# Optimization experiments

Hardware: AMD Instinct MI355X
Metric: run time of the kernel (lower is better)

Reference implementation:

```python
import jax, jax.numpy as jnp
import numpy as np

EMBED = 8      # embed_dim channels of 32-blade multivectors
HIDDEN = 32    # hidden_dim channels
BLADES = 32    # 2^5 Clifford blades
DT = 0.01


def setup_inputs() -> dict:
    key = jax.random.key(0)
    ks = jax.random.split(key, 8)
    B, S, N, D = 32, 256, 16, 6
    scale = lambda k, shape: jax.random.normal(k, shape, jnp.float32) * 0.1
    return {
        "x": jax.random.normal(ks[0], (B, S, N, D), jnp.float32),
        # input_proj: Linear(6, embed_dim*32)
        "W_in": scale(ks[1], (D, EMBED * BLADES)),
        "b_in": jnp.zeros((EMBED * BLADES,), jnp.float32),
        # VersorLinear(embed, hidden): channel-mixing weight shared across blades, per-blade bias
        "W1": scale(ks[2], (HIDDEN, EMBED)),
        "b1": scale(ks[3], (HIDDEN, BLADES)),
        "W2": scale(ks[4], (HIDDEN, HIDDEN)),
        "b2": scale(ks[5], (HIDDEN, BLADES)),
        "W3": scale(ks[6], (1, HIDDEN)),
        "b3": scale(ks[7], (1, BLADES)),
    }


def _versor_linear(h, W, b):
    # h: [..., in_ch, 32 blades]; mix channels, shared over blades
    return jnp.einsum('...ik,oi->...ok', h, W) + b


def _versor_act(h):
    # gate each multivector channel by sigmoid of its scalar (blade-0) part
    return h * jax.nn.sigmoid(h[..., 0:1])


def _energy(x_flat, W_in, b_in, W1, b1, W2, b2, W3, b3):
    BS, N, D = x_flat.shape
    h = x_flat @ W_in + b_in                    # [BS, N, EMBED*32]
    h = h.reshape(BS, N, EMBED, BLADES)         # [BS, N, embed, 32]
    h = _versor_act(_versor_linear(h, W1, b1))
    h = _versor_act(_versor_linear(h, W2, b2))
    h = _versor_linear(h, W3, b3)               # [BS, N, 1, 32]
    return h[..., 0].sum()                      # scalar energy


def reference(x, W_in, b_in, W1, b1, W2, b2, W3, b3):
    B, S, N, D = x.shape
    x_flat = x.reshape(B * S, N, D)
    # symplectic gradient of the Hamiltonian w.r.t. state
    grads = jax.grad(_energy)(x_flat, W_in, b_in, W1, b1, W2, b2, W3, b3)
    dq_dt = grads[..., 3:]
    dp_dt = -grads[..., :3]
    next_state = x_flat + jnp.concatenate([dq_dt, dp_dt], axis=-1) * DT
    return next_state.reshape(B, S, N, D)
```

## Files before the change

kernel.cpp:

```cpp
#include <hip/hip_runtime.h>
#include <hip/hip_bf16.h>

#define DT_STEP 0.01f

typedef __bf16 bf16x8 __attribute__((ext_vector_type(8)));
typedef float  f32x4  __attribute__((ext_vector_type(4)));

#define OFF_W2   0
#define OFF_W1   4096
#define OFF_WIND 5120
#define OFF_BIND 5312
#define OFF_B1D  5344
#define OFF_B2D  5472
#define OFF_W3   5600
#define OFF_WE   5728
#define OFF_BE   6496
#define OFF_WCP  6624
#define OFF_WAVE 7680
#define LDS_TOTAL (7680 + 4*3072)

__device__ __forceinline__ bf16x8 readT(const char* buf, int l15, int lhi) {
    return *(const bf16x8*)(buf + ((l15 * 64 + lhi * 16) ^ ((l15 & 7) << 4)));
}

__device__ __forceinline__ void act_sw(const f32x4& p0, const f32x4& p1,
                                       float* t0, float* t1, char* buf, int l15, int lhi) {
#pragma unroll
    for (int e = 0; e < 4; ++e) {
        int s = lhi * 4 + e, m = (s & 7) << 4;
        float a = p0[e], g = 1.f / (1.f + __expf(-a));
        t0[e] = g * fmaf(a, 1.f - g, 1.f);
        *(__bf16*)(buf + ((s * 64 + l15 * 2) ^ m)) = (__bf16)(a * g);
        a = p1[e]; g = 1.f / (1.f + __expf(-a));
        t1[e] = g * fmaf(a, 1.f - g, 1.f);
        *(__bf16*)(buf + ((s * 64 + (l15 + 16) * 2) ^ m)) = (__bf16)(a * g);
    }
}

__device__ __forceinline__ void d2_sw(const f32x4& p0, const f32x4& p1,
                                      float w30, float w31, char* buf, int l15, int lhi) {
#pragma unroll
    for (int e = 0; e < 4; ++e) {
        int s = lhi * 4 + e, m = (s & 7) << 4;
        float a = p0[e], g = 1.f / (1.f + __expf(-a));
        *(__bf16*)(buf + ((s * 64 + l15 * 2) ^ m)) = (__bf16)(w30 * g * fmaf(a, 1.f - g, 1.f));
        a = p1[e]; g = 1.f / (1.f + __expf(-a));
        *(__bf16*)(buf + ((s * 64 + (l15 + 16) * 2) ^ m)) = (__bf16)(w31 * g * fmaf(a, 1.f - g, 1.f));
    }
}

__device__ __forceinline__ void d1_sw(const f32x4& u0, const f32x4& u1,
                                      const float* t0, const float* t1, char* buf, int l15, int lhi) {
#pragma unroll
    for (int e = 0; e < 4; ++e) {
        int s = lhi * 4 + e, m = (s & 7) << 4;
        *(__bf16*)(buf + ((s * 64 + l15 * 2) ^ m))        = (__bf16)(u0[e] * t0[e]);
        *(__bf16*)(buf + ((s * 64 + (l15 + 16) * 2) ^ m)) = (__bf16)(u1[e] * t1[e]);
    }
}

__global__ __launch_bounds__(256) void hvnn_fused(
    const float* __restrict__ x,
    const float* __restrict__ Win, const float* __restrict__ bin,
    const float* __restrict__ W1,  const float* __restrict__ b1,
    const float* __restrict__ W2,  const float* __restrict__ b2,
    const float* __restrict__ W3,
    float* __restrict__ out, int ntiles)
{
    __shared__ __align__(16) char lds[LDS_TOTAL];
    const int tid = threadIdx.x;
    const int lane = tid & 63, wv = tid >> 6;
    const int l15 = lane & 15, lhi = lane >> 4;

    const int tileA = blockIdx.x * 8 + wv;
    const int tileB = tileA + 4;
    const bool vA = tileA < ntiles, vB = tileB < ntiles;

    char* wbase = lds + OFF_WAVE + wv * 3072;
    char* bufA = wbase;         char* bufB = wbase + 1024;
    char* xA   = wbase + 2048;  char* xB   = wbase + 2560;

    if (lane < 48) {
        if (vA) *(float2*)(xA + lane * 8) = ((const float2*)x)[(size_t)tileA * 48 + lane];
        if (vB) *(float2*)(xB + lane * 8) = ((const float2*)x)[(size_t)tileB * 48 + lane];
    }

    ((float4*)(lds + OFF_W2))[tid] = ((const float4*)W2)[tid];
    ((float*)(lds + OFF_W1))[tid]  = W1[tid];
    if (tid < 48) ((float*)(lds + OFF_WIND))[tid] = Win[(tid >> 3) * 256 + (tid & 7) * 32];
    if (tid < 8)  ((float*)(lds + OFF_BIND))[tid] = bin[tid * 32];
    if (tid < 32) ((float*)(lds + OFF_B1D))[tid]  = b1[tid * 32];
    if (tid < 32) ((float*)(lds + OFF_B2D))[tid]  = b2[tid * 32];
    if (tid < 32) ((float*)(lds + OFF_W3))[tid]   = W3[tid];
    __syncthreads();

    const float* W1s  = (const float*)(lds + OFF_W1);
    const float* Wind = (const float*)(lds + OFF_WIND);
    if (tid < 192) {
        int d = tid >> 5, o = tid & 31;
        float a = 0.f;
#pragma unroll
        for (int i = 0; i < 8; ++i) a = fmaf(Wind[d * 8 + i], W1s[o * 8 + i], a);
        ((float*)(lds + OFF_WE))[d * 32 + o] = a;
    }
    if (tid < 32) {
        float a = ((const float*)(lds + OFF_B1D))[tid];
#pragma unroll
        for (int i = 0; i < 8; ++i) a = fmaf(((const float*)(lds + OFF_BIND))[i], W1s[tid * 8 + i], a);
        ((float*)(lds + OFF_BE))[tid] = a;
    }
    {
        int o = tid >> 3, d = tid & 7;
        float v = 0.f;
        if (d < 6) {
            int dd = d < 3 ? d + 3 : d - 3;
            float sg = d < 3 ? 1.f : -1.f;
            float a = 0.f;
#pragma unroll
            for (int i = 0; i < 8; ++i) a = fmaf(W1s[o * 8 + i], Wind[dd * 8 + i], a);
            v = sg * a;
        }
        ((float*)(lds + OFF_WCP))[o * 8 + d] = v;
    }
    __syncthreads();

    const float* WeS  = (const float*)(lds + OFF_WE);
    const float* W2s  = (const float*)(lds + OFF_W2);
    const float* WcpS = (const float*)(lds + OFF_WCP);
    bf16x8 bwe0 = {}, bwe1 = {}, bw2t0, bw2t1, bw2b0, bw2b1, bwc = {};
    if (lane < 16) {
#pragma unroll
        for (int d = 0; d < 6; ++d) {
            bwe0[d] = (__bf16)WeS[d * 32 + l15];
            bwe1[d] = (__bf16)WeS[d * 32 + l15 + 16];
        }
    }
#pragma unroll
    for (int j = 0; j < 8; ++j) {
        bw2t0[j] = (__bf16)W2s[l15 * 32 + lhi * 8 + j];
        bw2t1[j] = (__bf16)W2s[(l15 + 16) * 32 + lhi * 8 + j];
        bw2b0[j] = (__bf16)W2s[(lhi * 8 + j) * 32 + l15];
        bw2b1[j] = (__bf16)W2s[(lhi * 8 + j) * 32 + l15 + 16];
    }
    if (l15 < 6) {
#pragma unroll
        for (int j = 0; j < 8; ++j) bwc[j] = (__bf16)WcpS[(lhi * 8 + j) * 8 + l15];
    }
    const float be0  = ((const float*)(lds + OFF_BE))[l15];
    const float be1  = ((const float*)(lds + OFF_BE))[l15 + 16];
    const float b2c0 = ((const float*)(lds + OFF_B2D))[l15];
    const float b2c1 = ((const float*)(lds + OFF_B2D))[l15 + 16];
    const float w3c0 = ((const float*)(lds + OFF_W3))[l15];
    const float w3c1 = ((const float*)(lds + OFF_W3))[l15 + 16];

    bf16x8 axA = {}, axB = {};
    if (lane < 16) {
        const float* ra = (const float*)(xA + lane * 24);
        const float* rb = (const float*)(xB + lane * 24);
#pragma unroll
        for (int d = 0; d < 6; ++d) { axA[d] = (__bf16)ra[d]; axB[d] = (__bf16)rb[d]; }
    }

    const f32x4 c0 = {be0, be0, be0, be0}, c1 = {be1, be1, be1, be1};
    f32x4 h1p0A = __builtin_amdgcn_mfma_f32_16x16x32_bf16(axA, bwe0, c0, 0, 0, 0);
    f32x4 h1p1A = __builtin_amdgcn_mfma_f32_16x16x32_bf16(axA, bwe1, c1, 0, 0, 0);
    f32x4 h1p0B = __builtin_amdgcn_mfma_f32_16x16x32_bf16(axB, bwe0, c0, 0, 0, 0);
    f32x4 h1p1B = __builtin_amdgcn_mfma_f32_16x16x32_bf16(axB, bwe1, c1, 0, 0, 0);

    float t10A[4], t11A[4], t10B[4], t11B[4];
    act_sw(h1p0A, h1p1A, t10A, t11A, bufA, l15, lhi);
    act_sw(h1p0B, h1p1B, t10B, t11B, bufB, l15, lhi);
    bf16x8 h1aA = readT(bufA, l15, lhi);
    bf16x8 h1aB = readT(bufB, l15, lhi);

    const f32x4 cb0 = {b2c0, b2c0, b2c0, b2c0}, cb1 = {b2c1, b2c1, b2c1, b2c1};
    f32x4 h2p0A = __builtin_amdgcn_mfma_f32_16x16x32_bf16(h1aA, bw2t0, cb0, 0, 0, 0);
    f32x4 h2p1A = __builtin_amdgcn_mfma_f32_16x16x32_bf16(h1aA, bw2t1, cb1, 0, 0, 0);
    f32x4 h2p0B = __builtin_amdgcn_mfma_f32_16x16x32_bf16(h1aB, bw2t0, cb0, 0, 0, 0);
    f32x4 h2p1B = __builtin_amdgcn_mfma_f32_16x16x32_bf16(h1aB, bw2t1, cb1, 0, 0, 0);

    d2_sw(h2p0A, h2p1A, w3c0, w3c1, bufA, l15, lhi);
    d2_sw(h2p0B, h2p1B, w3c0, w3c1, bufB, l15, lhi);
    bf16x8 d2aA = readT(bufA, l15, lhi);
    bf16x8 d2aB = readT(bufB, l15, lhi);

    const f32x4 z = {0.f, 0.f, 0.f, 0.f};
    f32x4 u10A = __builtin_amdgcn_mfma_f32_16x16x32_bf16(d2aA, bw2b0, z, 0, 0, 0);
    f32x4 u11A = __builtin_amdgcn_mfma_f32_16x16x32_bf16(d2aA, bw2b1, z, 0, 0, 0);
    f32x4 u10B = __builtin_amdgcn_mfma_f32_16x16x32_bf16(d2aB, bw2b0, z, 0, 0, 0);
    f32x4 u11B = __builtin_amdgcn_mfma_f32_16x16x32_bf16(d2aB, bw2b1, z, 0, 0, 0);

    d1_sw(u10A, u11A, t10A, t11A, bufA, l15, lhi);
    d1_sw(u10B, u11B, t10B, t11B, bufB, l15, lhi);
    bf16x8 d1aA = readT(bufA, l15, lhi);
    bf16x8 d1aB = readT(bufB, l15, lhi);

    f32x4 gxA = __builtin_amdgcn_mfma_f32_16x16x32_bf16(d1aA, bwc, z, 0, 0, 0);
    f32x4 gxB = __builtin_amdgcn_mfma_f32_16x16x32_bf16(d1aB, bwc, z, 0, 0, 0);

    if (l15 < 6) {
#pragma unroll
        for (int e = 0; e < 4; ++e) {
            int di = (lhi * 4 + e) * 6 + l15;
            *(float*)(bufA + di * 4) = fmaf(DT_STEP, gxA[e], *(const float*)(xA + di * 4));
            *(float*)(bufB + di * 4) = fmaf(DT_STEP, gxB[e], *(const float*)(xB + di * 4));
        }
    }
    if (lane < 48) {
        if (vA) ((float2*)out)[(size_t)tileA * 48 + lane] = *(const float2*)(bufA + lane * 8);
        if (vB) ((float2*)out)[(size_t)tileB * 48 + lane] = *(const float2*)(bufB + lane * 8);
    }
}

extern "C" void kernel_launch(void* const* d_in, const int* in_sizes, int n_in,
                              void* d_out, int out_size, void* d_ws, size_t ws_size,
                              hipStream_t stream) {
    const float* x    = (const float*)d_in[0];
    const float* W_in = (const float*)d_in[1];
    const float* b_in = (const float*)d_in[2];
    const float* W1   = (const float*)d_in[3];
    const float* b1   = (const float*)d_in[4];
    const float* W2   = (const float*)d_in[5];
    const float* b2   = (const float*)d_in[6];
    const float* W3   = (const float*)d_in[7];
    float* out = (float*)d_out;

    const int NS     = in_sizes[0] / 6;
    const int ntiles = NS / 16;
    const int blocks = (ntiles + 7) / 8;

    hvnn_fused<<<blocks, 256, 0, stream>>>(x, W_in, b_in, W1, b1, W2, b2, W3, out, ntiles);
}
```

Measured before the change: 16.65 us.

## Keep MFMA chain in registers via transposed operand order and four tiles per wave

Swaps the MFMA operand roles so that each layer's output accumulator layout directly matches the next layer's input operand layout, with channel permutation c1/c2. This removes the LDS transpose write/read round trips between layers. Each wave now processes four tiles (two chains of two), which halves the block count and amortizes the per-block weight setup. DT is folded into the coupling weights. The trade-off is fewer blocks, less parallelism across the GPU, and a longer serial chain per wave.

```diff
diff --git a/kernel.cpp b/kernel.cpp
--- a/kernel.cpp
+++ b/kernel.cpp
@@ -17,47 +17,7 @@
 #define OFF_BE   6496
 #define OFF_WCP  6624
 #define OFF_WAVE 7680
-#define LDS_TOTAL (7680 + 4*3072)
-
-__device__ __forceinline__ bf16x8 readT(const char* buf, int l15, int lhi) {
-    return *(const bf16x8*)(buf + ((l15 * 64 + lhi * 16) ^ ((l15 & 7) << 4)));
-}
-
-__device__ __forceinline__ void act_sw(const f32x4& p0, const f32x4& p1,
-                                       float* t0, float* t1, char* buf, int l15, int lhi) {
-#pragma unroll
-    for (int e = 0; e < 4; ++e) {
-        int s = lhi * 4 + e, m = (s & 7) << 4;
-        float a = p0[e], g = 1.f / (1.f + __expf(-a));
-        t0[e] = g * fmaf(a, 1.f - g, 1.f);
-        *(__bf16*)(buf + ((s * 64 + l15 * 2) ^ m)) = (__bf16)(a * g);
-        a = p1[e]; g = 1.f / (1.f + __expf(-a));
-        t1[e] = g * fmaf(a, 1.f - g, 1.f);
-        *(__bf16*)(buf + ((s * 64 + (l15 + 16) * 2) ^ m)) = (__bf16)(a * g);
-    }
-}
-
-__device__ __forceinline__ void d2_sw(const f32x4& p0, const f32x4& p1,
-                                      float w30, float w31, char* buf, int l15, int lhi) {
-#pragma unroll
-    for (int e = 0; e < 4; ++e) {
-        int s = lhi * 4 + e, m = (s & 7) << 4;
-        float a = p0[e], g = 1.f / (1.f + __expf(-a));
-        *(__bf16*)(buf + ((s * 64 + l15 * 2) ^ m)) = (__bf16)(w30 * g * fmaf(a, 1.f - g, 1.f));
-        a = p1[e]; g = 1.f / (1.f + __expf(-a));
-        *(__bf16*)(buf + ((s * 64 + (l15 + 16) * 2) ^ m)) = (__bf16)(w31 * g * fmaf(a, 1.f - g, 1.f));
-    }
-}
-
-__device__ __forceinline__ void d1_sw(const f32x4& u0, const f32x4& u1,
-                                      const float* t0, const float* t1, char* buf, int l15, int lhi) {
-#pragma unroll
-    for (int e = 0; e < 4; ++e) {
-        int s = lhi * 4 + e, m = (s & 7) << 4;
-        *(__bf16*)(buf + ((s * 64 + l15 * 2) ^ m))        = (__bf16)(u0[e] * t0[e]);
-        *(__bf16*)(buf + ((s * 64 + (l15 + 16) * 2) ^ m)) = (__bf16)(u1[e] * t1[e]);
-    }
-}
+#define LDS_TOTAL (7680 + 4*768)
 
 __global__ __launch_bounds__(256) void hvnn_fused(
     const float* __restrict__ x,
@@ -71,19 +31,8 @@
     const int tid = threadIdx.x;
     const int lane = tid & 63, wv = tid >> 6;
     const int l15 = lane & 15, lhi = lane >> 4;
-
-    const int tileA = blockIdx.x * 8 + wv;
-    const int tileB = tileA + 4;
-    const bool vA = tileA < ntiles, vB = tileB < ntiles;
-
-    char* wbase = lds + OFF_WAVE + wv * 3072;
-    char* bufA = wbase;         char* bufB = wbase + 1024;
-    char* xA   = wbase + 2048;  char* xB   = wbase + 2560;
-
-    if (lane < 48) {
-        if (vA) *(float2*)(xA + lane * 8) = ((const float2*)x)[(size_t)tileA * 48 + lane];
-        if (vB) *(float2*)(xB + lane * 8) = ((const float2*)x)[(size_t)tileB * 48 + lane];
-    }
+    const int wid = blockIdx.x * 4 + wv;
+    const int nwaves = gridDim.x * 4;
 
     ((float4*)(lds + OFF_W2))[tid] = ((const float4*)W2)[tid];
     ((float*)(lds + OFF_W1))[tid]  = W1[tid];
@@ -114,7 +63,7 @@
         float v = 0.f;
         if (d < 6) {
             int dd = d < 3 ? d + 3 : d - 3;
-            float sg = d < 3 ? 1.f : -1.f;
+            float sg = d < 3 ? DT_STEP : -DT_STEP;
             float a = 0.f;
 #pragma unroll
             for (int i = 0; i < 8; ++i) a = fmaf(W1s[o * 8 + i], Wind[dd * 8 + i], a);
@@ -127,89 +76,143 @@
     const float* WeS  = (const float*)(lds + OFF_WE);
     const float* W2s  = (const float*)(lds + OFF_W2);
     const float* WcpS = (const float*)(lds + OFF_WCP);
-    bf16x8 bwe0 = {}, bwe1 = {}, bw2t0, bw2t1, bw2b0, bw2b1, bwc = {};
-    if (lane < 16) {
+    const float* beS  = (const float*)(lds + OFF_BE);
+    const float* b2dS = (const float*)(lds + OFF_B2D);
+    const float* w3S  = (const float*)(lds + OFF_W3);
+    const int c1 = ((l15 >> 2) << 3) | (l15 & 3);
+    const int c2 = c1 + 4;
+
+    bf16x8 awe1 = {}, awe2 = {};
+    if (lhi == 0) {
 #pragma unroll
         for (int d = 0; d < 6; ++d) {
-            bwe0[d] = (__bf16)WeS[d * 32 + l15];
-            bwe1[d] = (__bf16)WeS[d * 32 + l15 + 16];
-        }
-    }
+            awe1[d] = (__bf16)WeS[d * 32 + c1];
+            awe2[d] = (__bf16)WeS[d * 32 + c2];
+        }
+    }
+    bf16x8 aw2f1, aw2f2, aw2b1, aw2b2;
 #pragma unroll
     for (int j = 0; j < 8; ++j) {
-        bw2t0[j] = (__bf16)W2s[l15 * 32 + lhi * 8 + j];
-        bw2t1[j] = (__bf16)W2s[(l15 + 16) * 32 + lhi * 8 + j];
-        bw2b0[j] = (__bf16)W2s[(lhi * 8 + j) * 32 + l15];
-        bw2b1[j] = (__bf16)W2s[(lhi * 8 + j) * 32 + l15 + 16];
-    }
+        aw2f1[j] = (__bf16)W2s[c1 * 32 + lhi * 8 + j];
+        aw2f2[j] = (__bf16)W2s[c2 * 32 + lhi * 8 + j];
+        aw2b1[j] = (__bf16)W2s[(lhi * 8 + j) * 32 + c1];
+        aw2b2[j] = (__bf16)W2s[(lhi * 8 + j) * 32 + c2];
+    }
+    bf16x8 awc = {};
     if (l15 < 6) {
 #pragma unroll
-        for (int j = 0; j < 8; ++j) bwc[j] = (__bf16)WcpS[(lhi * 8 + j) * 8 + l15];
-    }
-    const float be0  = ((const float*)(lds + OFF_BE))[l15];
-    const float be1  = ((const float*)(lds + OFF_BE))[l15 + 16];
-    const float b2c0 = ((const float*)(lds + OFF_B2D))[l15];
-    const float b2c1 = ((const float*)(lds + OFF_B2D))[l15 + 16];
-    const float w3c0 = ((const float*)(lds + OFF_W3))[l15];
-    const float w3c1 = ((const float*)(lds + OFF_W3))[l15 + 16];
-
-    bf16x8 axA = {}, axB = {};
-    if (lane < 16) {
-        const float* ra = (const float*)(xA + lane * 24);
-        const float* rb = (const float*)(xB + lane * 24);
-#pragma unroll
-        for (int d = 0; d < 6; ++d) { axA[d] = (__bf16)ra[d]; axB[d] = (__bf16)rb[d]; }
-    }
-
-    const f32x4 c0 = {be0, be0, be0, be0}, c1 = {be1, be1, be1, be1};
-    f32x4 h1p0A = __builtin_amdgcn_mfma_f32_16x16x32_bf16(axA, bwe0, c0, 0, 0, 0);
-    f32x4 h1p1A = __builtin_amdgcn_mfma_f32_16x16x32_bf16(axA, bwe1, c1, 0, 0, 0);
-    f32x4 h1p0B = __builtin_amdgcn_mfma_f32_16x16x32_bf16(axB, bwe0, c0, 0, 0, 0);
-    f32x4 h1p1B = __builtin_amdgcn_mfma_f32_16x16x32_bf16(axB, bwe1, c1, 0, 0, 0);
-
-    float t10A[4], t11A[4], t10B[4], t11B[4];
-    act_sw(h1p0A, h1p1A, t10A, t11A, bufA, l15, lhi);
-    act_sw(h1p0B, h1p1B, t10B, t11B, bufB, l15, lhi);
-    bf16x8 h1aA = readT(bufA, l15, lhi);
-    bf16x8 h1aB = readT(bufB, l15, lhi);
-
-    const f32x4 cb0 = {b2c0, b2c0, b2c0, b2c0}, cb1 = {b2c1, b2c1, b2c1, b2c1};
-    f32x4 h2p0A = __builtin_amdgcn_mfma_f32_16x16x32_bf16(h1aA, bw2t0, cb0, 0, 0, 0);
-    f32x4 h2p1A = __builtin_amdgcn_mfma_f32_16x16x32_bf16(h1aA, bw2t1, cb1, 0, 0, 0);
-    f32x4 h2p0B = __builtin_amdgcn_mfma_f32_16x16x32_bf16(h1aB, bw2t0, cb0, 0, 0, 0);
-    f32x4 h2p1B = __builtin_amdgcn_mfma_f32_16x16x32_bf16(h1aB, bw2t1, cb1, 0, 0, 0);
-
-    d2_sw(h2p0A, h2p1A, w3c0, w3c1, bufA, l15, lhi);
-    d2_sw(h2p0B, h2p1B, w3c0, w3c1, bufB, l15, lhi);
-    bf16x8 d2aA = readT(bufA, l15, lhi);
-    bf16x8 d2aB = readT(bufB, l15, lhi);
-
+        for (int j = 0; j < 8; ++j) awc[j] = (__bf16)WcpS[(lhi * 8 + j) * 8 + l15];
+    }
+    const f32x4 beC1 = *(const f32x4*)(beS + lhi * 8);
+    const f32x4 beC2 = *(const f32x4*)(beS + lhi * 8 + 4);
+    const f32x4 b2C1 = *(const f32x4*)(b2dS + lhi * 8);
+    const f32x4 b2C2 = *(const f32x4*)(b2dS + lhi * 8 + 4);
+    const f32x4 w3A  = *(const f32x4*)(w3S + lhi * 8);
+    const f32x4 w3B  = *(const f32x4*)(w3S + lhi * 8 + 4);
+
+    char* obufA = lds + OFF_WAVE + wv * 768;
+    char* obufB = obufA + 384;
     const f32x4 z = {0.f, 0.f, 0.f, 0.f};
-    f32x4 u10A = __builtin_amdgcn_mfma_f32_16x16x32_bf16(d2aA, bw2b0, z, 0, 0, 0);
-    f32x4 u11A = __builtin_amdgcn_mfma_f32_16x16x32_bf16(d2aA, bw2b1, z, 0, 0, 0);
-    f32x4 u10B = __builtin_amdgcn_mfma_f32_16x16x32_bf16(d2aB, bw2b0, z, 0, 0, 0);
-    f32x4 u11B = __builtin_amdgcn_mfma_f32_16x16x32_bf16(d2aB, bw2b1, z, 0, 0, 0);
-
-    d1_sw(u10A, u11A, t10A, t11A, bufA, l15, lhi);
-    d1_sw(u10B, u11B, t10B, t11B, bufB, l15, lhi);
-    bf16x8 d1aA = readT(bufA, l15, lhi);
-    bf16x8 d1aB = readT(bufB, l15, lhi);
-
-    f32x4 gxA = __builtin_amdgcn_mfma_f32_16x16x32_bf16(d1aA, bwc, z, 0, 0, 0);
-    f32x4 gxB = __builtin_amdgcn_mfma_f32_16x16x32_bf16(d1aB, bwc, z, 0, 0, 0);
-
-    if (l15 < 6) {
+
+    auto chain = [&](bool vA, bool vB, int tA, int tB,
+                     float2 xa0, float2 xa1, float2 xa2,
+                     float2 xb0, float2 xb1, float2 xb2) {
+        bf16x8 bxA = {}, bxB = {};
+        if (lhi == 0) {
+            bxA[0] = (__bf16)xa0.x; bxA[1] = (__bf16)xa0.y; bxA[2] = (__bf16)xa1.x;
+            bxA[3] = (__bf16)xa1.y; bxA[4] = (__bf16)xa2.x; bxA[5] = (__bf16)xa2.y;
+            bxB[0] = (__bf16)xb0.x; bxB[1] = (__bf16)xb0.y; bxB[2] = (__bf16)xb1.x;
+            bxB[3] = (__bf16)xb1.y; bxB[4] = (__bf16)xb2.x; bxB[5] = (__bf16)xb2.y;
+        }
+        f32x4 h1A1 = __builtin_amdgcn_mfma_f32_16x16x32_bf16(awe1, bxA, beC1, 0, 0, 0);
+        f32x4 h1A2 = __builtin_amdgcn_mfma_f32_16x16x32_bf16(awe2, bxA, beC2, 0, 0, 0);
+        f32x4 h1B1 = __builtin_amdgcn_mfma_f32_16x16x32_bf16(awe1, bxB, beC1, 0, 0, 0);
+        f32x4 h1B2 = __builtin_amdgcn_mfma_f32_16x16x32_bf16(awe2, bxB, beC2, 0, 0, 0);
+        bf16x8 h1fA, h1fB; float t1A1[4], t1A2[4], t1B1[4], t1B2[4];
 #pragma unroll
         for (int e = 0; e < 4; ++e) {
-            int di = (lhi * 4 + e) * 6 + l15;
-            *(float*)(bufA + di * 4) = fmaf(DT_STEP, gxA[e], *(const float*)(xA + di * 4));
-            *(float*)(bufB + di * 4) = fmaf(DT_STEP, gxB[e], *(const float*)(xB + di * 4));
-        }
-    }
-    if (lane < 48) {
-        if (vA) ((float2*)out)[(size_t)tileA * 48 + lane] = *(const float2*)(bufA + lane * 8);
-        if (vB) ((float2*)out)[(size_t)tileB * 48 + lane] = *(const float2*)(bufB + lane * 8);
-    }
+            float a, g;
+            a = h1A1[e]; g = 1.f / (1.f + __expf(-a));
+            t1A1[e] = g * fmaf(a, 1.f - g, 1.f); h1fA[e] = (__bf16)(a * g);
+            a = h1A2[e]; g = 1.f / (1.f + __expf(-a));
+            t1A2[e] = g * fmaf(a, 1.f - g, 1.f); h1fA[e + 4] = (__bf16)(a * g);
+            a = h1B1[e]; g = 1.f / (1.f + __expf(-a));
+            t1B1[e] = g * fmaf(a, 1.f - g, 1.f); h1fB[e] = (__bf16)(a * g);
+            a = h1B2[e]; g = 1.f / (1.f + __expf(-a));
+            t1B2[e] = g * fmaf(a, 1.f - g, 1.f); h1fB[e + 4] = (__bf16)(a * g);
+        }
+        f32x4 h2A1 = __builtin_amdgcn_mfma_f32_16x16x32_bf16(aw2f1, h1fA, b2C1, 0, 0, 0);
+        f32x4 h2A2 = __builtin_amdgcn_mfma_f32_16x16x32_bf16(aw2f2, h1fA, b2C2, 0, 0, 0);
+        f32x4 h2B1 = __builtin_amdgcn_mfma_f32_16x16x32_bf16(aw2f1, h1fB, b2C1, 0, 0, 0);
+        f32x4 h2B2 = __builtin_amdgcn_mfma_f32_16x16x32_bf16(aw2f2, h1fB, b2C2, 0, 0, 0);
+        bf16x8 d2fA, d2fB;
+#pragma unroll
+        for (int e = 0; e < 4; ++e) {
+            float a, g;
+            a = h2A1[e]; g = 1.f / (1.f + __expf(-a));
+            d2fA[e]     = (__bf16)(w3A[e] * g * fmaf(a, 1.f - g, 1.f));
+            a = h2A2[e]; g = 1.f / (1.f + __expf(-a));
+            d2fA[e + 4] = (__bf16)(w3B[e] * g * fmaf(a, 1.f - g, 1.f));
+            a = h2B1[e]; g = 1.f / (1.f + __expf(-a));
+            d2fB[e]     = (__bf16)(w3A[e] * g * fmaf(a, 1.f - g, 1.f));
+            a = h2B2[e]; g = 1.f / (1.f + __expf(-a));
+            d2fB[e + 4] = (__bf16)(w3B[e] * g * fmaf(a, 1.f - g, 1.f));
+        }
+        f32x4 u1A1 = __builtin_amdgcn_mfma_f32_16x16x32_bf16(aw2b1, d2fA, z, 0, 0, 0);
+        f32x4 u1A2 = __builtin_amdgcn_mfma_f32_16x16x32_bf16(aw2b2, d2fA, z, 0, 0, 0);
+        f32x4 u1B1 = __builtin_amdgcn_mfma_f32_16x16x32_bf16(aw2b1, d2fB, z, 0, 0, 0);
+        f32x4 u1B2 = __builtin_amdgcn_mfma_f32_16x16x32_bf16(aw2b2, d2fB, z, 0, 0, 0);
+        bf16x8 d1fA, d1fB;
+#pragma unroll
+        for (int e = 0; e < 4; ++e) {
+            d1fA[e]     = (__bf16)(u1A1[e] * t1A1[e]);
+            d1fA[e + 4] = (__bf16)(u1A2[e] * t1A2[e]);
+            d1fB[e]     = (__bf16)(u1B1[e] * t1B1[e]);
+            d1fB[e + 4] = (__bf16)(u1B2[e] * t1B2[e]);
+        }
+        f32x4 gxA = __builtin_amdgcn_mfma_f32_16x16x32_bf16(awc, d1fA, z, 0, 0, 0);
+        f32x4 gxB = __builtin_amdgcn_mfma_f32_16x16x32_bf16(awc, d1fB, z, 0, 0, 0);
+
+        if (lhi < 2) {
+#pragma unroll
+            for (int e = 0; e < 4; ++e) {
+                int d = lhi * 4 + e;
+                if (d < 6) {
+                    *(float*)(obufA + l15 * 24 + d * 4) = gxA[e];
+                    *(float*)(obufB + l15 * 24 + d * 4) = gxB[e];
+                }
+            }
+        }
+        if (lane < 48) {
+            if (vA) {
+                float2 xv = ((const float2*)x)[(size_t)tA * 48 + lane];
+                float2 g2 = *(const float2*)(obufA + lane * 8);
+                ((float2*)out)[(size_t)tA * 48 + lane] = make_float2(xv.x + g2.x, xv.y + g2.y);
+            }
+            if (vB) {
+                float2 xv = ((const float2*)x)[(size_t)tB * 48 + lane];
+                float2 g2 = *(const float2*)(obufB + lane * 8);
+                ((float2*)out)[(size_t)tB * 48 + lane] = make_float2(xv.x + g2.x, xv.y + g2.y);
+            }
+        }
+    };
+
+    const int p0 = wid, p1 = nwaves + wid;
+    const int tA0 = 2 * p0, tB0 = 2 * p0 + 1, tA1 = 2 * p1, tB1 = 2 * p1 + 1;
+    const bool vA0 = tA0 < ntiles, vB0 = tB0 < ntiles;
+    const bool vA1 = tA1 < ntiles, vB1 = tB1 < ntiles;
+
+    float2 a00 = {}, a01 = {}, a02 = {}, b00 = {}, b01 = {}, b02 = {};
+    float2 a10 = {}, a11 = {}, a12 = {}, b10 = {}, b11 = {}, b12 = {};
+    if (lhi == 0) {
+        const float2* xf2 = (const float2*)x;
+        if (vA0) { const float2* p = xf2 + (size_t)tA0 * 48 + l15 * 3; a00 = p[0]; a01 = p[1]; a02 = p[2]; }
+        if (vB0) { const float2* p = xf2 + (size_t)tB0 * 48 + l15 * 3; b00 = p[0]; b01 = p[1]; b02 = p[2]; }
+        if (vA1) { const float2* p = xf2 + (size_t)tA1 * 48 + l15 * 3; a10 = p[0]; a11 = p[1]; a12 = p[2]; }
+        if (vB1) { const float2* p = xf2 + (size_t)tB1 * 48 + l15 * 3; b10 = p[0]; b11 = p[1]; b12 = p[2]; }
+    }
+    chain(vA0, vB0, tA0, tB0, a00, a01, a02, b00, b01, b02);
+    chain(vA1, vB1, tA1, tB1, a10, a11, a12, b10, b11, b12);
 }
 
 extern "C" void kernel_launch(void* const* d_in, const int* in_sizes, int n_in,
@@ -226,8 +229,8 @@
     float* out = (float*)d_out;
 
     const int NS     = in_sizes[0] / 6;
-    const int ntiles = NS / 16;
-    const int blocks = (ntiles + 7) / 8;
+    const int ntiles = (NS + 15) / 16;
+    const int blocks = (ntiles + 15) / 16;
 
     hvnn_fused<<<blocks, 256, 0, stream>>>(x, W_in, b_in, W1, b1, W2, b2, W3, out, ntiles);
 }
```

Result: faster. 15.38 us (-7.6%).
